# Performance work log

Hardware: AMD Instinct MI355X
Metric: run time of the kernel (lower is better)

The kernel has to match this reference:

```python
import jax, jax.numpy as jnp
import numpy as np

# Problem sizes
N = 131072      # total nodes (B graphs x 256 nodes)
E = 1048576     # total edges (avg degree 8)
V = 30000       # vocab
D = 128         # emb_size
H = 128         # hidden_size
T = 4           # num edge types; edge_to_id['ne'] == 0
L = 2           # num RGCN layers
B = 512         # num graphs in batch
PPG = 32        # predicate nodes per graph (uniform G_sizes)
IN_FEATS = D + 5  # emb + spo(3) + access(1) + pre_access(1)


def setup_inputs() -> dict:
    key = jax.random.key(0)
    ks = jax.random.split(key, 14)
    npg = N // B  # nodes per graph
    # predicate nodes: first PPG nodes of each graph (so G_sizes = [PPG]*B)
    pred_idx = (jnp.arange(B)[:, None] * npg + jnp.arange(PPG)[None, :]).reshape(-1)
    global_id = jax.random.randint(ks[0], (N,), 2, V)
    spo = jnp.zeros((N, 3), jnp.int32).at[pred_idx, 1].set(1)
    so = jax.random.randint(ks[1], (N, 2), 0, 2).astype(jnp.int32)
    notp = 1 - spo[:, 1]
    spo = spo.at[:, 0].set(so[:, 0] * notp).at[:, 2].set(so[:, 1] * notp)
    access = jax.random.randint(ks[2], (N, 1), 0, 5).astype(jnp.int32)
    pre_access = jax.random.randint(ks[3], (N, 1), 0, 5).astype(jnp.int32)
    src = jax.random.randint(ks[4], (E,), 0, N)
    dst = jax.random.randint(ks[5], (E,), 0, N)
    etype = jax.random.randint(ks[6], (E,), 0, T)
    norm = jax.random.uniform(ks[7], (E, 1), dtype=jnp.float32)
    # parameters
    emb_table = (0.02 * jax.random.normal(ks[8], (V, D), jnp.float32)).at[:2].set(0.0)
    W_t = 0.05 * jax.random.normal(ks[9], (IN_FEATS, H), jnp.float32)
    b_t = jnp.zeros((H,), jnp.float32)
    W_r = 0.05 * jax.random.normal(ks[10], (L, T, H, H), jnp.float32)
    b_r = jnp.zeros((L, H), jnp.float32)
    Wb = 0.05 * jax.random.normal(ks[11], (H, H), jnp.float32)
    bb = jnp.zeros((), jnp.float32)
    return {"emb_table": emb_table, "W_t": W_t, "b_t": b_t, "W_r": W_r,
            "b_r": b_r, "Wb": Wb, "bb": bb, "norm": norm,
            "global_id": global_id, "spo": spo, "access": access,
            "pre_access": pre_access, "src": src, "dst": dst,
            "etype": etype, "pred_idx": pred_idx}


def reference(emb_table, W_t, b_t, W_r, b_r, Wb, bb, norm,
              global_id, spo, access, pre_access, src, dst, etype, pred_idx):
    seg = lambda m, idx: jax.ops.segment_sum(m, idx, num_segments=N)
    # --- init_forward: send/recv over 'ne' edges, update only ne nodes with messages ---
    emb = emb_table[global_id]                                  # [N, D]
    ne = (etype == 0).astype(emb.dtype)[:, None]                # edge_to_id['ne'] == 0
    agg0 = seg(emb[src] * norm * ne, dst)                       # mailbox sum
    deg = seg(ne[:, 0], dst)
    is_ne = (spo[:, 0] + spo[:, 2]) > 0
    emb = jnp.where((is_ne & (deg > 0))[:, None], agg0, emb)
    # --- input projection ---
    h = jnp.concatenate([emb, spo.astype(emb.dtype), access.astype(emb.dtype),
                         pre_access.astype(emb.dtype)], axis=1) @ W_t + b_t  # [N, H]
    prev = h
    # --- RGCN layers: per-edge-type W, message = (h_src @ W_t) * norm, scatter-sum ---
    for l in range(L):
        agg = jnp.zeros((N, H), h.dtype)
        for t in range(T):
            mask_t = (etype == t).astype(h.dtype)[:, None]
            agg = agg + seg((h @ W_r[l, t])[src] * norm * mask_t, dst)
        h = jax.nn.relu(agg + b_r[l])
        if l != L - 1:  # residual, skipped on last layer as in source
            h = h + prev
            prev = h
    # --- predict: segment-mean pooling (equivalent to block-diag proj matmul) + bilinear ---
    hp = h[pred_idx].reshape(B, PPG, H)
    pool = hp.mean(axis=1)                                      # [B, H]
    out = jnp.einsum('bph,hk,bk->bp', hp, Wb, pool) + bb        # nn.Bilinear(H, H, 1)
    return jax.nn.log_softmax(out, axis=1).reshape(-1)          # per-graph log_softmax
```

## Files before the change

kernel.cpp:

```cpp
#include <hip/hip_runtime.h>
#include <hip/hip_bf16.h>

#define N_NODES 131072
#define N_EDGES 1048576
#define HID 128
#define NB 512
#define PPG 32
#define NKEYS (4 * N_NODES)
#define NTILES (NKEYS / 256)
#define KPROJ 160
#define KLAY  512

typedef short bf16x8 __attribute__((ext_vector_type(8)));
typedef float f32x4  __attribute__((ext_vector_type(4)));
typedef unsigned int u32x4 __attribute__((ext_vector_type(4)));

__device__ __forceinline__ float bf2f(unsigned short u) {
    return __uint_as_float(((unsigned int)u) << 16);
}
__device__ __forceinline__ unsigned short f2bf(float x) {
    unsigned int u = __float_as_uint(x);
    unsigned int r = ((u >> 16) & 1u) + 0x7fffu;
    return (unsigned short)((u + r) >> 16);
}
__device__ __forceinline__ unsigned int pack2(float a, float b) {
    return (unsigned int)f2bf(a) | ((unsigned int)f2bf(b) << 16);
}

__global__ void count_kernel(const int* __restrict__ dst, const int* __restrict__ etype,
                             int* __restrict__ rp) {
    int e = blockIdx.x * blockDim.x + threadIdx.x;
    if (e >= N_EDGES) return;
    atomicAdd(rp + etype[e] * N_NODES + dst[e], 1);
}

__global__ void scan_tile_kernel(int* __restrict__ rp, int* __restrict__ tsum) {
    __shared__ int s[256];
    int g = blockIdx.x * 256 + threadIdx.x;
    int v = rp[g];
    s[threadIdx.x] = v;
    __syncthreads();
    for (int off = 1; off < 256; off <<= 1) {
        int tv = (threadIdx.x >= off) ? s[threadIdx.x - off] : 0;
        __syncthreads();
        s[threadIdx.x] += tv;
        __syncthreads();
    }
    rp[g] = s[threadIdx.x] - v;
    if (threadIdx.x == 255) tsum[blockIdx.x] = s[255];
}

__global__ void scan_tsum_kernel(int* __restrict__ tsum) {
    __shared__ int s[256];
    int t = threadIdx.x;
    int loc[8]; int sum = 0;
#pragma unroll
    for (int i = 0; i < 8; ++i) { loc[i] = tsum[t * 8 + i]; sum += loc[i]; }
    s[t] = sum;
    __syncthreads();
    for (int off = 1; off < 256; off <<= 1) {
        int tv = (t >= off) ? s[t - off] : 0;
        __syncthreads();
        s[t] += tv;
        __syncthreads();
    }
    int run = s[t] - sum;
#pragma unroll
    for (int i = 0; i < 8; ++i) { int v = loc[i]; tsum[t * 8 + i] = run; run += v; }
}

__global__ void scan_add_kernel(int* __restrict__ rp, const int* __restrict__ tsum) {
    int g = blockIdx.x * 256 + threadIdx.x;
    rp[g] += tsum[g >> 8];
}

__global__ void scatter_kernel(const int* __restrict__ src, const int* __restrict__ dst,
                               const int* __restrict__ etype, const float* __restrict__ norm,
                               int* __restrict__ rp, int2* __restrict__ erec) {
    int e = blockIdx.x * blockDim.x + threadIdx.x;
    if (e >= N_EDGES) return;
    int key = etype[e] * N_NODES + dst[e];
    int pos = atomicAdd(rp + key, 1);
    erec[pos] = make_int2(src[e], __float_as_int(norm[e]));
}

__global__ void wtrans_kernel(const float* __restrict__ W_t, const float* __restrict__ W_r,
                              unsigned short* __restrict__ WTp, unsigned short* __restrict__ WTl) {
    int u = blockIdx.x * 256 + threadIdx.x;
    if (u < 2560) {
        int c = u / 20, k0 = (u % 20) * 8;
#pragma unroll
        for (int j = 0; j < 8; ++j) {
            int k = k0 + j;
            float v = (k < 133) ? W_t[k * HID + c] : 0.f;
            WTp[c * KPROJ + k] = f2bf(v);
        }
    } else if (u < 2560 + 16384) {
        int v = u - 2560;
        int l = v / 8192; int rr = v % 8192;
        int c = rr / 64; int k0 = (rr % 64) * 8;
#pragma unroll
        for (int j = 0; j < 8; ++j) {
            int k = k0 + j; int t = k >> 7; int i = k & 127;
            float w = W_r[(((size_t)(l * 4 + t) * HID) + i) * HID + c];
            WTl[((size_t)l * HID + c) * KLAY + k] = f2bf(w);
        }
    }
}

__global__ __launch_bounds__(256) void prep_kernel(
        const int* __restrict__ rp, const int2* __restrict__ erec,
        const int* __restrict__ gid,
        const int* __restrict__ spo, const int* __restrict__ access,
        const int* __restrict__ pre, const float* __restrict__ emb,
        unsigned short* __restrict__ A0) {
    int wave = threadIdx.x >> 6, lane = threadIdx.x & 63;
    int n = blockIdx.x * 4 + wave;
    int g = lane >> 5, sl = lane & 31;
    int s0 = spo[n * 3], s1 = spo[n * 3 + 1], s2 = spo[n * 3 + 2];
    int rb = n ? rp[n - 1] : 0, re = rp[n];
    float a0 = 0.f, a1 = 0.f, a2 = 0.f, a3 = 0.f;
    if ((s0 + s2) > 0 && re > rb) {
        for (int i = rb + g; i < re; i += 2) {
            int2 er = erec[i];
            float nm = __int_as_float(er.y);
            float4 v = ((const float4*)(emb + (size_t)gid[er.x] * HID))[sl];
            a0 += v.x * nm; a1 += v.y * nm; a2 += v.z * nm; a3 += v.w * nm;
        }
        a0 += __shfl_xor(a0, 32, 64);
        a1 += __shfl_xor(a1, 32, 64);
        a2 += __shfl_xor(a2, 32, 64);
        a3 += __shfl_xor(a3, 32, 64);
    } else if (g == 0) {
        float4 v = ((const float4*)(emb + (size_t)gid[n] * HID))[sl];
        a0 = v.x; a1 = v.y; a2 = v.z; a3 = v.w;
    }
    unsigned int* row = (unsigned int*)(A0 + (size_t)n * KPROJ);
    if (g == 0) {
        uint2 o; o.x = pack2(a0, a1); o.y = pack2(a2, a3);
        *(uint2*)(row + sl * 2) = o;
    }
    if (lane < 16) {
        int c0 = 128 + lane * 2;
        float f0 = 0.f, f1 = 0.f;
        if (c0 == 128)      { f0 = (float)s0;      f1 = (float)s1; }
        else if (c0 == 130) { f0 = (float)s2;      f1 = (float)access[n]; }
        else if (c0 == 132) { f0 = (float)pre[n];  f1 = 0.f; }
        row[64 + lane] = pack2(f0, f1);
    }
}

__device__ __forceinline__ void acc8(float* a, u32x4 v, float nm) {
    a[0] = fmaf(bf2f((unsigned short)(v.x & 0xffffu)), nm, a[0]);
    a[1] = fmaf(bf2f((unsigned short)(v.x >> 16)),     nm, a[1]);
    a[2] = fmaf(bf2f((unsigned short)(v.y & 0xffffu)), nm, a[2]);
    a[3] = fmaf(bf2f((unsigned short)(v.y >> 16)),     nm, a[3]);
    a[4] = fmaf(bf2f((unsigned short)(v.z & 0xffffu)), nm, a[4]);
    a[5] = fmaf(bf2f((unsigned short)(v.z >> 16)),     nm, a[5]);
    a[6] = fmaf(bf2f((unsigned short)(v.w & 0xffffu)), nm, a[6]);
    a[7] = fmaf(bf2f((unsigned short)(v.w >> 16)),     nm, a[7]);
}

__global__ __launch_bounds__(256) void agg_kernel(
        const int* __restrict__ rp, const int2* __restrict__ erec,
        const unsigned short* __restrict__ hb, unsigned short* __restrict__ Aagg) {
    int wave = threadIdx.x >> 6, lane = threadIdx.x & 63;
    int d = blockIdx.x * 4 + wave;
    int t = lane >> 4, sl = lane & 15;
    int key = t * N_NODES + d;
    int rb = key ? rp[key - 1] : 0;
    int re = rp[key];
    float a[8] = {0.f, 0.f, 0.f, 0.f, 0.f, 0.f, 0.f, 0.f};
    int i = rb;
    for (; i + 2 <= re; i += 2) {
        int2 e0 = erec[i];
        int2 e1 = erec[i + 1];
        u32x4 v0 = *((const u32x4*)(hb + (size_t)e0.x * HID) + sl);
        u32x4 v1 = *((const u32x4*)(hb + (size_t)e1.x * HID) + sl);
        acc8(a, v0, __int_as_float(e0.y));
        acc8(a, v1, __int_as_float(e1.y));
    }
    if (i < re) {
        int2 e0 = erec[i];
        u32x4 v0 = *((const u32x4*)(hb + (size_t)e0.x * HID) + sl);
        acc8(a, v0, __int_as_float(e0.y));
    }
    u32x4 o;
    o.x = pack2(a[0], a[1]); o.y = pack2(a[2], a[3]);
    o.z = pack2(a[4], a[5]); o.w = pack2(a[6], a[7]);
    __builtin_nontemporal_store(o, (u32x4*)(Aagg + (size_t)d * KLAY + t * HID) + sl);
}

__device__ __forceinline__ void stage_tile(const unsigned short* gbase, int ldK,
                                           int k0, int bk, unsigned short* lds,
                                           int wid, int lane) {
    int iters = bk >> 4;
    int sh = (bk == 64) ? 3 : 2;
    int msk = (1 << sh) - 1;
    int swz = (bk == 64) ? 7 : 3;
    for (int i = 0; i < iters; ++i) {
        int c = (i * 4 + wid) * 64 + lane;
        int row = c >> sh, cc = c & msk;
        int ccg = cc ^ (row & swz);
        const unsigned short* g = gbase + (size_t)row * ldK + k0 + ccg * 8;
        unsigned short* l = lds + (size_t)(i * 4 + wid) * 512;
        __builtin_amdgcn_global_load_lds(
            (const __attribute__((address_space(1))) void*)g,
            (__attribute__((address_space(3))) void*)l, 16, 0, 0);
    }
}

__global__ __launch_bounds__(256) void gemm_kernel(
        const unsigned short* __restrict__ A, int K,
        const unsigned short* __restrict__ WT, const float* __restrict__ bias,
        unsigned short* __restrict__ hb, int mode) {
    __shared__ unsigned short At[128 * 64];
    __shared__ unsigned short Bt[128 * 64];
    int tid = threadIdx.x;
    int base = blockIdx.x * 128;
    int wid = tid >> 6, lane = tid & 63;
    int wr = wid >> 1, wc = wid & 1;
    int lr = lane & 15, g16 = lane >> 4;
    f32x4 acc[4][4];
#pragma unroll
    for (int m = 0; m < 4; ++m)
#pragma unroll
        for (int n = 0; n < 4; ++n) { acc[m][n][0] = 0.f; acc[m][n][1] = 0.f; acc[m][n][2] = 0.f; acc[m][n][3] = 0.f; }
    const unsigned short* Abase = A + (size_t)base * K;
    for (int k0 = 0; k0 < K; k0 += 64) {
        int bk = K - k0; if (bk > 64) bk = 64;
        int swz = (bk == 64) ? 7 : 3;
        __syncthreads();
        stage_tile(Abase, K, k0, bk, At, wid, lane);
        stage_tile(WT,    K, k0, bk, Bt, wid, lane);
        __syncthreads();
        int ks = bk >> 5;
        for (int kk = 0; kk < ks; ++kk) {
            bf16x8 a[4], b[4];
            int cc = kk * 4 + g16;
#pragma unroll
            for (int m = 0; m < 4; ++m) {
                int ar = wr * 64 + m * 16 + lr;
                a[m] = *(const bf16x8*)&At[ar * bk + ((cc ^ (ar & swz)) << 3)];
            }
#pragma unroll
            for (int n = 0; n < 4; ++n) {
                int br = wc * 64 + n * 16 + lr;
                b[n] = *(const bf16x8*)&Bt[br * bk + ((cc ^ (br & swz)) << 3)];
            }
#pragma unroll
            for (int m = 0; m < 4; ++m)
#pragma unroll
                for (int n = 0; n < 4; ++n)
                    acc[m][n] = __builtin_amdgcn_mfma_f32_16x16x32_bf16(a[m], b[n], acc[m][n], 0, 0, 0);
        }
    }
    float bcol[4];
#pragma unroll
    for (int n = 0; n < 4; ++n) bcol[n] = bias[wc * 64 + n * 16 + lr];
    int r0g = (lane >> 4) * 4;
#pragma unroll
    for (int m = 0; m < 4; ++m) {
        int row = base + wr * 64 + m * 16 + r0g;
#pragma unroll
        for (int n = 0; n < 4; ++n) {
            int col = wc * 64 + n * 16 + lr;
#pragma unroll
            for (int r = 0; r < 4; ++r) {
                float v = acc[m][n][r] + bcol[n];
                size_t idx = (size_t)(row + r) * HID + col;
                if (mode == 1)      v = fmaxf(v, 0.f) + bf2f(hb[idx]);
                else if (mode == 2) v = fmaxf(v, 0.f);
                hb[idx] = f2bf(v);
            }
        }
    }
}

__global__ void predict_kernel(const unsigned short* __restrict__ hb,
                               const int* __restrict__ pred_idx,
                               const float* __restrict__ Wb, const float* __restrict__ bbp,
                               float* __restrict__ out) {
    int b = blockIdx.x;
    int tid = threadIdx.x;
    __shared__ float hp[PPG * HID];
    __shared__ float pool[HID];
    __shared__ float vv[HID];
    __shared__ float sc[PPG];
    __shared__ float lse;
    for (int k = tid; k < PPG * HID; k += 256) {
        int p = k >> 7, j = k & 127;
        int node = pred_idx[b * PPG + p];
        hp[k] = bf2f(hb[(size_t)node * HID + j]);
    }
    __syncthreads();
    if (tid < HID) {
        float s = 0.f;
        for (int p = 0; p < PPG; ++p) s += hp[p * HID + tid];
        pool[tid] = s * (1.0f / PPG);
    }
    __syncthreads();
    if (tid < HID) {
        float s = 0.f;
        for (int k = 0; k < HID; ++k) s += Wb[tid * HID + k] * pool[k];
        vv[tid] = s;
    }
    __syncthreads();
    if (tid < PPG) {
        float s = bbp[0];
        for (int j = 0; j < HID; ++j) s += hp[tid * HID + j] * vv[j];
        sc[tid] = s;
    }
    __syncthreads();
    if (tid == 0) {
        float m = -INFINITY;
        for (int p = 0; p < PPG; ++p) m = fmaxf(m, sc[p]);
        float se = 0.f;
        for (int p = 0; p < PPG; ++p) se += expf(sc[p] - m);
        lse = m + logf(se);
    }
    __syncthreads();
    if (tid < PPG) out[b * PPG + tid] = sc[tid] - lse;
}

extern "C" void kernel_launch(void* const* d_in, const int* in_sizes, int n_in,
                              void* d_out, int out_size, void* d_ws, size_t ws_size,
                              hipStream_t stream) {
    const float* emb_table  = (const float*)d_in[0];
    const float* W_t        = (const float*)d_in[1];
    const float* b_t        = (const float*)d_in[2];
    const float* W_r        = (const float*)d_in[3];
    const float* b_r        = (const float*)d_in[4];
    const float* Wb         = (const float*)d_in[5];
    const float* bb         = (const float*)d_in[6];
    const float* norm       = (const float*)d_in[7];
    const int*   global_id  = (const int*)d_in[8];
    const int*   spo        = (const int*)d_in[9];
    const int*   access     = (const int*)d_in[10];
    const int*   pre_access = (const int*)d_in[11];
    const int*   src        = (const int*)d_in[12];
    const int*   dst        = (const int*)d_in[13];
    const int*   etype      = (const int*)d_in[14];
    const int*   pred_idx   = (const int*)d_in[15];
    float* out = (float*)d_out;

    char* ws = (char*)d_ws;
    size_t off = 0;
    unsigned short* hb   = (unsigned short*)(ws + off); off += (size_t)N_NODES * HID * 2;
    unsigned short* Abuf = (unsigned short*)(ws + off); off += (size_t)N_NODES * KLAY * 2;
    int*   rp    = (int*)(ws + off);   off += (size_t)NKEYS * 4;
    int*   tsum  = (int*)(ws + off);   off += (size_t)NTILES * 4;
    int2*  erec  = (int2*)(ws + off);  off += (size_t)N_EDGES * 8;
    unsigned short* WTp = (unsigned short*)(ws + off); off += (size_t)HID * KPROJ * 2;
    unsigned short* WTl = (unsigned short*)(ws + off); off += (size_t)2 * HID * KLAY * 2;
    unsigned short* A0 = Abuf;

    hipMemsetAsync(rp, 0, (size_t)NKEYS * 4, stream);
    count_kernel<<<N_EDGES / 256, 256, 0, stream>>>(dst, etype, rp);
    scan_tile_kernel<<<NTILES, 256, 0, stream>>>(rp, tsum);
    scan_tsum_kernel<<<1, 256, 0, stream>>>(tsum);
    scan_add_kernel<<<NTILES, 256, 0, stream>>>(rp, tsum);
    scatter_kernel<<<N_EDGES / 256, 256, 0, stream>>>(src, dst, etype, norm, rp, erec);

    wtrans_kernel<<<74, 256, 0, stream>>>(W_t, W_r, WTp, WTl);

    prep_kernel<<<N_NODES / 4, 256, 0, stream>>>(rp, erec, global_id, spo,
                                                 access, pre_access, emb_table, A0);
    gemm_kernel<<<N_NODES / 128, 256, 0, stream>>>(A0, KPROJ, WTp, b_t, hb, 0);

    agg_kernel<<<N_NODES / 4, 256, 0, stream>>>(rp, erec, hb, Abuf);
    gemm_kernel<<<N_NODES / 128, 256, 0, stream>>>(Abuf, KLAY, WTl, b_r, hb, 1);
    agg_kernel<<<N_NODES / 4, 256, 0, stream>>>(rp, erec, hb, Abuf);
    gemm_kernel<<<N_NODES / 128, 256, 0, stream>>>(Abuf, KLAY, WTl + (size_t)HID * KLAY,
                                                   b_r + HID, hb, 2);

    predict_kernel<<<NB, 256, 0, stream>>>(hb, pred_idx, Wb, bb, out);
}
```

Before: 535.7 us.

## Transform node features per edge type before aggregating, with a dst-only CSR

The layers now first compute h @ W_r[t] for all four edge types into a 4×N×H buffer, then gather and sum those rows along a CSR keyed only by destination. This replaces the old order of aggregating into an N×512 buffer and then running a K=512 GEMM. The edge type is packed into the high bits of the source index, so one sorted edge list serves all types. Bias, ReLU and residual are fused into the aggregation kernel, and the layer GEMM launches are removed. In exchange, the per-edge gathers now read from a table four times larger than the old hidden-state buffer, which may hurt cache locality.

```diff
diff --git a/kernel.cpp b/kernel.cpp
--- a/kernel.cpp
+++ b/kernel.cpp
@@ -6,8 +6,7 @@
 #define HID 128
 #define NB 512
 #define PPG 32
-#define NKEYS (4 * N_NODES)
-#define NTILES (NKEYS / 256)
+#define NTILES_D (N_NODES / 256)
 #define KPROJ 160
 #define KLAY  512
 
@@ -27,11 +26,10 @@
     return (unsigned int)f2bf(a) | ((unsigned int)f2bf(b) << 16);
 }
 
-__global__ void count_kernel(const int* __restrict__ dst, const int* __restrict__ etype,
-                             int* __restrict__ rp) {
+__global__ void count_kernel(const int* __restrict__ dst, int* __restrict__ rp) {
     int e = blockIdx.x * blockDim.x + threadIdx.x;
     if (e >= N_EDGES) return;
-    atomicAdd(rp + etype[e] * N_NODES + dst[e], 1);
+    atomicAdd(rp + dst[e], 1);
 }
 
 __global__ void scan_tile_kernel(int* __restrict__ rp, int* __restrict__ tsum) {
@@ -53,9 +51,9 @@
 __global__ void scan_tsum_kernel(int* __restrict__ tsum) {
     __shared__ int s[256];
     int t = threadIdx.x;
-    int loc[8]; int sum = 0;
-#pragma unroll
-    for (int i = 0; i < 8; ++i) { loc[i] = tsum[t * 8 + i]; sum += loc[i]; }
+    int loc[2]; int sum = 0;
+#pragma unroll
+    for (int i = 0; i < 2; ++i) { loc[i] = tsum[t * 2 + i]; sum += loc[i]; }
     s[t] = sum;
     __syncthreads();
     for (int off = 1; off < 256; off <<= 1) {
@@ -66,7 +64,7 @@
     }
     int run = s[t] - sum;
 #pragma unroll
-    for (int i = 0; i < 8; ++i) { int v = loc[i]; tsum[t * 8 + i] = run; run += v; }
+    for (int i = 0; i < 2; ++i) { int v = loc[i]; tsum[t * 2 + i] = run; run += v; }
 }
 
 __global__ void scan_add_kernel(int* __restrict__ rp, const int* __restrict__ tsum) {
@@ -79,9 +77,8 @@
                                int* __restrict__ rp, int2* __restrict__ erec) {
     int e = blockIdx.x * blockDim.x + threadIdx.x;
     if (e >= N_EDGES) return;
-    int key = etype[e] * N_NODES + dst[e];
-    int pos = atomicAdd(rp + key, 1);
-    erec[pos] = make_int2(src[e], __float_as_int(norm[e]));
+    int pos = atomicAdd(rp + dst[e], 1);
+    erec[pos] = make_int2(src[e] | (etype[e] << 17), __float_as_int(norm[e]));
 }
 
 __global__ void wtrans_kernel(const float* __restrict__ W_t, const float* __restrict__ W_r,
@@ -118,22 +115,32 @@
     int n = blockIdx.x * 4 + wave;
     int g = lane >> 5, sl = lane & 31;
     int s0 = spo[n * 3], s1 = spo[n * 3 + 1], s2 = spo[n * 3 + 2];
-    int rb = n ? rp[n - 1] : 0, re = rp[n];
     float a0 = 0.f, a1 = 0.f, a2 = 0.f, a3 = 0.f;
-    if ((s0 + s2) > 0 && re > rb) {
+    int cnt = 0;
+    bool isne = (s0 + s2) > 0;
+    if (isne) {
+        int rb = n ? rp[n - 1] : 0, re = rp[n];
         for (int i = rb + g; i < re; i += 2) {
             int2 er = erec[i];
-            float nm = __int_as_float(er.y);
-            float4 v = ((const float4*)(emb + (size_t)gid[er.x] * HID))[sl];
-            a0 += v.x * nm; a1 += v.y * nm; a2 += v.z * nm; a3 += v.w * nm;
+            if (((er.x >> 17) & 3) == 0) {
+                int s = er.x & 0x1FFFF;
+                float nm = __int_as_float(er.y);
+                float4 v = ((const float4*)(emb + (size_t)gid[s] * HID))[sl];
+                a0 += v.x * nm; a1 += v.y * nm; a2 += v.z * nm; a3 += v.w * nm;
+                cnt++;
+            }
         }
         a0 += __shfl_xor(a0, 32, 64);
         a1 += __shfl_xor(a1, 32, 64);
         a2 += __shfl_xor(a2, 32, 64);
         a3 += __shfl_xor(a3, 32, 64);
-    } else if (g == 0) {
-        float4 v = ((const float4*)(emb + (size_t)gid[n] * HID))[sl];
-        a0 = v.x; a1 = v.y; a2 = v.z; a3 = v.w;
+        cnt += __shfl_xor(cnt, 32, 64);
+    }
+    if (!isne || cnt == 0) {
+        if (g == 0) {
+            float4 v = ((const float4*)(emb + (size_t)gid[n] * HID))[sl];
+            a0 = v.x; a1 = v.y; a2 = v.z; a3 = v.w;
+        }
     }
     unsigned int* row = (unsigned int*)(A0 + (size_t)n * KPROJ);
     if (g == 0) {
@@ -147,6 +154,149 @@
         else if (c0 == 130) { f0 = (float)s2;      f1 = (float)access[n]; }
         else if (c0 == 132) { f0 = (float)pre[n];  f1 = 0.f; }
         row[64 + lane] = pack2(f0, f1);
+    }
+}
+
+__device__ __forceinline__ void stage_tile(const unsigned short* gbase, int ldK,
+                                           int k0, int bk, unsigned short* lds,
+                                           int wid, int lane) {
+    int iters = bk >> 4;
+    int sh = (bk == 128) ? 4 : ((bk == 64) ? 3 : 2);
+    int msk = (1 << sh) - 1;
+    for (int i = 0; i < iters; ++i) {
+        int c = (i * 4 + wid) * 64 + lane;
+        int row = c >> sh, cc = c & msk;
+        int ccg = cc ^ (row & msk);
+        const unsigned short* g = gbase + (size_t)row * ldK + k0 + ccg * 8;
+        unsigned short* l = lds + (size_t)(i * 4 + wid) * 512;
+        __builtin_amdgcn_global_load_lds(
+            (const __attribute__((address_space(1))) void*)g,
+            (__attribute__((address_space(3))) void*)l, 16, 0, 0);
+    }
+}
+
+__global__ __launch_bounds__(256) void gemm_kernel(
+        const unsigned short* __restrict__ A, int K,
+        const unsigned short* __restrict__ WT, const float* __restrict__ bias,
+        unsigned short* __restrict__ hb) {
+    __shared__ unsigned short At[128 * 64];
+    __shared__ unsigned short Bt[128 * 64];
+    int tid = threadIdx.x;
+    int base = blockIdx.x * 128;
+    int wid = tid >> 6, lane = tid & 63;
+    int wr = wid >> 1, wc = wid & 1;
+    int lr = lane & 15, g16 = lane >> 4;
+    f32x4 acc[4][4];
+#pragma unroll
+    for (int m = 0; m < 4; ++m)
+#pragma unroll
+        for (int n = 0; n < 4; ++n) { acc[m][n][0] = 0.f; acc[m][n][1] = 0.f; acc[m][n][2] = 0.f; acc[m][n][3] = 0.f; }
+    const unsigned short* Abase = A + (size_t)base * K;
+    for (int k0 = 0; k0 < K; k0 += 64) {
+        int bk = K - k0; if (bk > 64) bk = 64;
+        int swz = (bk == 64) ? 7 : 3;
+        __syncthreads();
+        stage_tile(Abase, K, k0, bk, At, wid, lane);
+        stage_tile(WT,    K, k0, bk, Bt, wid, lane);
+        __syncthreads();
+        int ks = bk >> 5;
+        for (int kk = 0; kk < ks; ++kk) {
+            bf16x8 a[4], b[4];
+            int cc = kk * 4 + g16;
+#pragma unroll
+            for (int m = 0; m < 4; ++m) {
+                int ar = wr * 64 + m * 16 + lr;
+                a[m] = *(const bf16x8*)&At[ar * bk + ((cc ^ (ar & swz)) << 3)];
+            }
+#pragma unroll
+            for (int n = 0; n < 4; ++n) {
+                int br = wc * 64 + n * 16 + lr;
+                b[n] = *(const bf16x8*)&Bt[br * bk + ((cc ^ (br & swz)) << 3)];
+            }
+#pragma unroll
+            for (int m = 0; m < 4; ++m)
+#pragma unroll
+                for (int n = 0; n < 4; ++n)
+                    acc[m][n] = __builtin_amdgcn_mfma_f32_16x16x32_bf16(a[m], b[n], acc[m][n], 0, 0, 0);
+        }
+    }
+    float bcol[4];
+#pragma unroll
+    for (int n = 0; n < 4; ++n) bcol[n] = bias[wc * 64 + n * 16 + lr];
+    int r0g = (lane >> 4) * 4;
+#pragma unroll
+    for (int m = 0; m < 4; ++m) {
+        int row = base + wr * 64 + m * 16 + r0g;
+#pragma unroll
+        for (int n = 0; n < 4; ++n) {
+            int col = wc * 64 + n * 16 + lr;
+#pragma unroll
+            for (int r = 0; r < 4; ++r)
+                hb[(size_t)(row + r) * HID + col] = f2bf(acc[m][n][r] + bcol[n]);
+        }
+    }
+}
+
+__global__ __launch_bounds__(256) void xt4_kernel(
+        const unsigned short* __restrict__ hb,
+        const unsigned short* __restrict__ WTlayer,
+        unsigned short* __restrict__ XT) {
+    __shared__ unsigned short Ah[128 * 128];
+    __shared__ unsigned short Bt[128 * 128];
+    int tid = threadIdx.x;
+    int base = blockIdx.x * 128;
+    int wid = tid >> 6, lane = tid & 63;
+    int wr = wid >> 1, wc = wid & 1;
+    int lr = lane & 15, g16 = lane >> 4;
+    int r0g = (lane >> 4) * 4;
+
+    stage_tile(hb + (size_t)base * HID, HID, 0, 128, Ah, wid, lane);
+    stage_tile(WTlayer, KLAY, 0, 128, Bt, wid, lane);
+    __syncthreads();
+
+    for (int t = 0; t < 4; ++t) {
+        f32x4 acc[4][4];
+#pragma unroll
+        for (int m = 0; m < 4; ++m)
+#pragma unroll
+            for (int n = 0; n < 4; ++n) { acc[m][n][0] = 0.f; acc[m][n][1] = 0.f; acc[m][n][2] = 0.f; acc[m][n][3] = 0.f; }
+#pragma unroll
+        for (int kk = 0; kk < 4; ++kk) {
+            bf16x8 a[4], b[4];
+            int cc = kk * 4 + g16;
+#pragma unroll
+            for (int m = 0; m < 4; ++m) {
+                int ar = wr * 64 + m * 16 + lr;
+                a[m] = *(const bf16x8*)&Ah[ar * 128 + ((cc ^ (ar & 15)) << 3)];
+            }
+#pragma unroll
+            for (int n = 0; n < 4; ++n) {
+                int br = wc * 64 + n * 16 + lr;
+                b[n] = *(const bf16x8*)&Bt[br * 128 + ((cc ^ (br & 15)) << 3)];
+            }
+#pragma unroll
+            for (int m = 0; m < 4; ++m)
+#pragma unroll
+                for (int n = 0; n < 4; ++n)
+                    acc[m][n] = __builtin_amdgcn_mfma_f32_16x16x32_bf16(a[m], b[n], acc[m][n], 0, 0, 0);
+        }
+        unsigned short* XTt = XT + ((size_t)t << 17) * HID;
+#pragma unroll
+        for (int m = 0; m < 4; ++m) {
+            int row = base + wr * 64 + m * 16 + r0g;
+#pragma unroll
+            for (int n = 0; n < 4; ++n) {
+                int col = wc * 64 + n * 16 + lr;
+#pragma unroll
+                for (int r = 0; r < 4; ++r)
+                    XTt[(size_t)(row + r) * HID + col] = f2bf(acc[m][n][r]);
+            }
+        }
+        if (t < 3) {
+            __syncthreads();
+            stage_tile(WTlayer, KLAY, (t + 1) * HID, 128, Bt, wid, lane);
+            __syncthreads();
+        }
     }
 }
 
@@ -163,117 +313,46 @@
 
 __global__ __launch_bounds__(256) void agg_kernel(
         const int* __restrict__ rp, const int2* __restrict__ erec,
-        const unsigned short* __restrict__ hb, unsigned short* __restrict__ Aagg) {
+        const unsigned short* __restrict__ XT, const float* __restrict__ bias,
+        unsigned short* __restrict__ hb, int residual) {
     int wave = threadIdx.x >> 6, lane = threadIdx.x & 63;
     int d = blockIdx.x * 4 + wave;
-    int t = lane >> 4, sl = lane & 15;
-    int key = t * N_NODES + d;
-    int rb = key ? rp[key - 1] : 0;
-    int re = rp[key];
+    int g = lane >> 4, sl = lane & 15;
+    int rb = d ? rp[d - 1] : 0;
+    int re = rp[d];
     float a[8] = {0.f, 0.f, 0.f, 0.f, 0.f, 0.f, 0.f, 0.f};
-    int i = rb;
-    for (; i + 2 <= re; i += 2) {
-        int2 e0 = erec[i];
-        int2 e1 = erec[i + 1];
-        u32x4 v0 = *((const u32x4*)(hb + (size_t)e0.x * HID) + sl);
-        u32x4 v1 = *((const u32x4*)(hb + (size_t)e1.x * HID) + sl);
-        acc8(a, v0, __int_as_float(e0.y));
-        acc8(a, v1, __int_as_float(e1.y));
-    }
-    if (i < re) {
-        int2 e0 = erec[i];
-        u32x4 v0 = *((const u32x4*)(hb + (size_t)e0.x * HID) + sl);
-        acc8(a, v0, __int_as_float(e0.y));
-    }
-    u32x4 o;
-    o.x = pack2(a[0], a[1]); o.y = pack2(a[2], a[3]);
-    o.z = pack2(a[4], a[5]); o.w = pack2(a[6], a[7]);
-    __builtin_nontemporal_store(o, (u32x4*)(Aagg + (size_t)d * KLAY + t * HID) + sl);
-}
-
-__device__ __forceinline__ void stage_tile(const unsigned short* gbase, int ldK,
-                                           int k0, int bk, unsigned short* lds,
-                                           int wid, int lane) {
-    int iters = bk >> 4;
-    int sh = (bk == 64) ? 3 : 2;
-    int msk = (1 << sh) - 1;
-    int swz = (bk == 64) ? 7 : 3;
-    for (int i = 0; i < iters; ++i) {
-        int c = (i * 4 + wid) * 64 + lane;
-        int row = c >> sh, cc = c & msk;
-        int ccg = cc ^ (row & swz);
-        const unsigned short* g = gbase + (size_t)row * ldK + k0 + ccg * 8;
-        unsigned short* l = lds + (size_t)(i * 4 + wid) * 512;
-        __builtin_amdgcn_global_load_lds(
-            (const __attribute__((address_space(1))) void*)g,
-            (__attribute__((address_space(3))) void*)l, 16, 0, 0);
-    }
-}
-
-__global__ __launch_bounds__(256) void gemm_kernel(
-        const unsigned short* __restrict__ A, int K,
-        const unsigned short* __restrict__ WT, const float* __restrict__ bias,
-        unsigned short* __restrict__ hb, int mode) {
-    __shared__ unsigned short At[128 * 64];
-    __shared__ unsigned short Bt[128 * 64];
-    int tid = threadIdx.x;
-    int base = blockIdx.x * 128;
-    int wid = tid >> 6, lane = tid & 63;
-    int wr = wid >> 1, wc = wid & 1;
-    int lr = lane & 15, g16 = lane >> 4;
-    f32x4 acc[4][4];
-#pragma unroll
-    for (int m = 0; m < 4; ++m)
-#pragma unroll
-        for (int n = 0; n < 4; ++n) { acc[m][n][0] = 0.f; acc[m][n][1] = 0.f; acc[m][n][2] = 0.f; acc[m][n][3] = 0.f; }
-    const unsigned short* Abase = A + (size_t)base * K;
-    for (int k0 = 0; k0 < K; k0 += 64) {
-        int bk = K - k0; if (bk > 64) bk = 64;
-        int swz = (bk == 64) ? 7 : 3;
-        __syncthreads();
-        stage_tile(Abase, K, k0, bk, At, wid, lane);
-        stage_tile(WT,    K, k0, bk, Bt, wid, lane);
-        __syncthreads();
-        int ks = bk >> 5;
-        for (int kk = 0; kk < ks; ++kk) {
-            bf16x8 a[4], b[4];
-            int cc = kk * 4 + g16;
-#pragma unroll
-            for (int m = 0; m < 4; ++m) {
-                int ar = wr * 64 + m * 16 + lr;
-                a[m] = *(const bf16x8*)&At[ar * bk + ((cc ^ (ar & swz)) << 3)];
-            }
-#pragma unroll
-            for (int n = 0; n < 4; ++n) {
-                int br = wc * 64 + n * 16 + lr;
-                b[n] = *(const bf16x8*)&Bt[br * bk + ((cc ^ (br & swz)) << 3)];
-            }
-#pragma unroll
-            for (int m = 0; m < 4; ++m)
-#pragma unroll
-                for (int n = 0; n < 4; ++n)
-                    acc[m][n] = __builtin_amdgcn_mfma_f32_16x16x32_bf16(a[m], b[n], acc[m][n], 0, 0, 0);
-        }
-    }
-    float bcol[4];
-#pragma unroll
-    for (int n = 0; n < 4; ++n) bcol[n] = bias[wc * 64 + n * 16 + lr];
-    int r0g = (lane >> 4) * 4;
-#pragma unroll
-    for (int m = 0; m < 4; ++m) {
-        int row = base + wr * 64 + m * 16 + r0g;
-#pragma unroll
-        for (int n = 0; n < 4; ++n) {
-            int col = wc * 64 + n * 16 + lr;
-#pragma unroll
-            for (int r = 0; r < 4; ++r) {
-                float v = acc[m][n][r] + bcol[n];
-                size_t idx = (size_t)(row + r) * HID + col;
-                if (mode == 1)      v = fmaxf(v, 0.f) + bf2f(hb[idx]);
-                else if (mode == 2) v = fmaxf(v, 0.f);
-                hb[idx] = f2bf(v);
-            }
-        }
+    for (int i = rb + g; i < re; i += 4) {
+        int2 er = erec[i];
+        int st = er.x;
+        float nm = __int_as_float(er.y);
+        u32x4 v = *((const u32x4*)(XT + (size_t)(st & 0x7FFFF) * HID) + sl);
+        acc8(a, v, nm);
+    }
+#pragma unroll
+    for (int k = 0; k < 8; ++k) {
+        a[k] += __shfl_xor(a[k], 16, 64);
+        a[k] += __shfl_xor(a[k], 32, 64);
+    }
+    if (g == 0) {
+        float r[8];
+#pragma unroll
+        for (int j = 0; j < 8; ++j) r[j] = fmaxf(a[j] + bias[sl * 8 + j], 0.f);
+        unsigned short* hrow = hb + (size_t)d * HID;
+        if (residual) {
+            u32x4 hv = *((const u32x4*)hrow + sl);
+            r[0] += bf2f((unsigned short)(hv.x & 0xffffu));
+            r[1] += bf2f((unsigned short)(hv.x >> 16));
+            r[2] += bf2f((unsigned short)(hv.y & 0xffffu));
+            r[3] += bf2f((unsigned short)(hv.y >> 16));
+            r[4] += bf2f((unsigned short)(hv.z & 0xffffu));
+            r[5] += bf2f((unsigned short)(hv.z >> 16));
+            r[6] += bf2f((unsigned short)(hv.w & 0xffffu));
+            r[7] += bf2f((unsigned short)(hv.w >> 16));
+        }
+        u32x4 o;
+        o.x = pack2(r[0], r[1]); o.y = pack2(r[2], r[3]);
+        o.z = pack2(r[4], r[5]); o.w = pack2(r[6], r[7]);
+        *((u32x4*)hrow + sl) = o;
     }
 }
 
@@ -346,33 +425,32 @@
 
     char* ws = (char*)d_ws;
     size_t off = 0;
-    unsigned short* hb   = (unsigned short*)(ws + off); off += (size_t)N_NODES * HID * 2;
-    unsigned short* Abuf = (unsigned short*)(ws + off); off += (size_t)N_NODES * KLAY * 2;
-    int*   rp    = (int*)(ws + off);   off += (size_t)NKEYS * 4;
-    int*   tsum  = (int*)(ws + off);   off += (size_t)NTILES * 4;
+    unsigned short* hb  = (unsigned short*)(ws + off); off += (size_t)N_NODES * HID * 2;
+    unsigned short* XT  = (unsigned short*)(ws + off); off += (size_t)4 * N_NODES * HID * 2;
+    int*   rp    = (int*)(ws + off);   off += (size_t)N_NODES * 4;
+    int*   tsum  = (int*)(ws + off);   off += (size_t)NTILES_D * 4;
     int2*  erec  = (int2*)(ws + off);  off += (size_t)N_EDGES * 8;
     unsigned short* WTp = (unsigned short*)(ws + off); off += (size_t)HID * KPROJ * 2;
     unsigned short* WTl = (unsigned short*)(ws + off); off += (size_t)2 * HID * KLAY * 2;
-    unsigned short* A0 = Abuf;
-
-    hipMemsetAsync(rp, 0, (size_t)NKEYS * 4, stream);
-    count_kernel<<<N_EDGES / 256, 256, 0, stream>>>(dst, etype, rp);
-    scan_tile_kernel<<<NTILES, 256, 0, stream>>>(rp, tsum);
+    unsigned short* A0 = XT;
+
+    hipMemsetAsync(rp, 0, (size_t)N_NODES * 4, stream);
+    count_kernel<<<N_EDGES / 256, 256, 0, stream>>>(dst, rp);
+    scan_tile_kernel<<<NTILES_D, 256, 0, stream>>>(rp, tsum);
     scan_tsum_kernel<<<1, 256, 0, stream>>>(tsum);
-    scan_add_kernel<<<NTILES, 256, 0, stream>>>(rp, tsum);
+    scan_add_kernel<<<NTILES_D, 256, 0, stream>>>(rp, tsum);
     scatter_kernel<<<N_EDGES / 256, 256, 0, stream>>>(src, dst, etype, norm, rp, erec);
 
     wtrans_kernel<<<74, 256, 0, stream>>>(W_t, W_r, WTp, WTl);
 
     prep_kernel<<<N_NODES / 4, 256, 0, stream>>>(rp, erec, global_id, spo,
                                                  access, pre_access, emb_table, A0);
-    gemm_kernel<<<N_NODES / 128, 256, 0, stream>>>(A0, KPROJ, WTp, b_t, hb, 0);
-
-    agg_kernel<<<N_NODES / 4, 256, 0, stream>>>(rp, erec, hb, Abuf);
-    gemm_kernel<<<N_NODES / 128, 256, 0, stream>>>(Abuf, KLAY, WTl, b_r, hb, 1);
-    agg_kernel<<<N_NODES / 4, 256, 0, stream>>>(rp, erec, hb, Abuf);
-    gemm_kernel<<<N_NODES / 128, 256, 0, stream>>>(Abuf, KLAY, WTl + (size_t)HID * KLAY,
-                                                   b_r + HID, hb, 2);
+    gemm_kernel<<<N_NODES / 128, 256, 0, stream>>>(A0, KPROJ, WTp, b_t, hb);
+
+    xt4_kernel<<<N_NODES / 128, 256, 0, stream>>>(hb, WTl, XT);
+    agg_kernel<<<N_NODES / 4, 256, 0, stream>>>(rp, erec, XT, b_r, hb, 1);
+    xt4_kernel<<<N_NODES / 128, 256, 0, stream>>>(hb, WTl + (size_t)HID * KLAY, XT);
+    agg_kernel<<<N_NODES / 4, 256, 0, stream>>>(rp, erec, XT, b_r + HID, hb, 0);
 
     predict_kernel<<<NB, 256, 0, stream>>>(hb, pred_idx, Wb, bb, out);
 }
```

Result: faster. 509.7 us (-4.9%).
